# Kernel optimization log

Hardware: AMD Instinct MI355X
Metric: run time of the kernel (lower is better)

Reference implementation:

```python
import jax, jax.numpy as jnp
import numpy as np

N = 20000      # atoms
E = 320000     # edges
G = 16         # graphs
NEL = 4        # chemical elements
M0 = 64        # 0e channels
M1 = 32        # 1o channels
NB = 8         # Bessel basis
L = 2          # conv layers
HID = 64       # radial MLP hidden
RMAX = 4.0
RIN = RMAX - 0.5
NNB = 16.0     # n_neighbors normalization


def _bessel(r):
    # Bessel radial embedding with smooth cosine cutoff between RIN and RMAX
    r_safe = jnp.maximum(r, 1e-6)
    n = jnp.arange(1, NB + 1, dtype=r.dtype)
    f = jnp.sqrt(2.0 / RMAX) * jnp.sin(n[None, :] * jnp.pi * r_safe[:, None] / RMAX) / r_safe[:, None]
    t = (r - RIN) / (RMAX - RIN)
    env = jnp.where(r < RIN, 1.0, jnp.where(r > RMAX, 0.0, 0.5 * (jnp.cos(jnp.pi * t) + 1.0)))
    return f * env[:, None]


def _conv(s, v, attrs, sh0, sh1, src, dst, remb, Wscs, Wscv, W1s, W1v, R0, R1, R2, W2s, W2v):
    # self-connection: FC tensor product of node features with scalar species attrs
    sc_s = jnp.einsum('ni,ne,ieo->no', s, attrs, Wscs) / np.sqrt(M0 * NEL)    # [N, M0+M1]
    sc_v = jnp.einsum('nic,ne,ieo->noc', v, attrs, Wscv) / np.sqrt(M1 * NEL)  # [N, M1, 3]
    # irrep-wise linear (channel mixing)
    s1 = s @ W1s / np.sqrt(M0)
    v1 = jnp.einsum('nic,io->noc', v, W1v) / np.sqrt(M1)
    # gather to edges
    se, ve = s1[src], v1[src]
    # radial MLP -> per-edge tensor-product weights (2*M0 + 2*M1 = 192)
    w = jax.nn.silu(remb @ R0 / np.sqrt(NB))
    w = jax.nn.silu(w @ R1 / np.sqrt(HID))
    w = w @ R2 / np.sqrt(HID)
    w1, w2, w3, w4 = w[:, :M0], w[:, M0:2 * M0], w[:, 2 * M0:2 * M0 + M1], w[:, 2 * M0 + M1:]
    # CG tensor product paths (uvu): 0e*0e->0e, 1o*1o->0e, 0e*1o->1o, 1o*0e->1o
    m_s = jnp.concatenate([
        w1 * se * sh0[:, None],
        w4 * jnp.einsum('eic,ec->ei', ve, sh1) / np.sqrt(3.0),
    ], axis=1)                                                   # [E, M0+M1]
    m_v = jnp.concatenate([
        (w2 * se)[:, :, None] * sh1[:, None, :],
        (w3 * sh0[:, None])[:, :, None] * ve,
    ], axis=1)                                                   # [E, M0+M1, 3]
    # scatter-sum aggregation
    a_s = jax.ops.segment_sum(m_s, dst, num_segments=N) / np.sqrt(NNB)
    a_v = jax.ops.segment_sum(m_v, dst, num_segments=N) / np.sqrt(NNB)
    # linear back to hidden irreps (+ gate scalars) and self-connection
    o_s = a_s @ W2s / np.sqrt(M0 + M1) + sc_s                    # [N, M0+M1]
    o_v = jnp.einsum('nic,io->noc', a_v, W2v) / np.sqrt(M0 + M1) + sc_v
    # gate nonlinearity: silu on scalars, silu-gates on vectors
    gate = jax.nn.silu(o_s[:, M0:])
    return jax.nn.silu(o_s[:, :M0]), o_v * gate[:, :, None]


def _forward(nodes, dR, senders, receivers, n_node, W_embed, W_sc_s, W_sc_v, W_l1_s, W_l1_v,
             Wr0, Wr1, Wr2, W_l2_s, W_l2_v, W_en1, W_en2, W_mag1, W_mag2,
             scale_occ, shift_occ, energy_scale, energy_shift):
    r = jnp.linalg.norm(dR, axis=-1)
    u = dR / jnp.maximum(r, 1e-6)[:, None]
    sh0 = jnp.ones_like(r)                 # Y0 (component norm)
    sh1 = np.sqrt(3.0) * u                 # Y1 (component norm)
    remb = _bessel(r)                      # [E, NB]
    s = nodes @ W_embed / np.sqrt(NEL)     # initial scalar embedding
    v = jnp.zeros((N, M1, 3), dtype=s.dtype)
    for l in range(L):
        s, v = _conv(s, v, nodes, sh0, sh1, senders, receivers, remb,
                     W_sc_s[l], W_sc_v[l], W_l1_s[l], W_l1_v[l],
                     Wr0[l], Wr1[l], Wr2[l], W_l2_s[l], W_l2_v[l])
    # energy readout
    h_en = s @ W_en1 / np.sqrt(M0)
    atomic = h_en @ W_en2 / np.sqrt(M0 // 2)
    atomic = energy_scale * atomic + energy_shift
    gidx = jnp.repeat(jnp.arange(G), n_node, total_repeat_length=N)
    energy = jax.ops.segment_sum(atomic, gidx, num_segments=G)   # [G, 1]
    # magnetization readout
    h_mag = s @ W_mag1 / np.sqrt(M0)
    mags = h_mag @ W_mag2 / np.sqrt(M0 // 2)                     # [N, 2]
    mags = (nodes[:, :-1] @ scale_occ) * mags + (nodes[:, :-1] @ shift_occ)
    return energy, mags


def setup_inputs() -> dict:
    key = jax.random.key(0)
    ks = jax.random.split(key, 30)
    f = jnp.float32
    inp = {
        'nodes': jax.random.uniform(ks[0], (N, NEL), dtype=f),
        'dR': jax.random.normal(ks[1], (E, 3), dtype=f),
        'senders': jax.random.randint(ks[2], (E,), 0, N, dtype=jnp.int32),
        'receivers': jax.random.randint(ks[3], (E,), 0, N, dtype=jnp.int32),
        'n_node': jnp.full((G,), N // G, dtype=jnp.int32),
        'W_embed': jax.random.normal(ks[4], (NEL, M0), dtype=f),
        'W_sc_s': jax.random.normal(ks[5], (L, M0, NEL, M0 + M1), dtype=f),
        'W_sc_v': jax.random.normal(ks[6], (L, M1, NEL, M1), dtype=f),
        'W_l1_s': jax.random.normal(ks[7], (L, M0, M0), dtype=f),
        'W_l1_v': jax.random.normal(ks[8], (L, M1, M1), dtype=f),
        'Wr0': jax.random.normal(ks[9], (L, NB, HID), dtype=f),
        'Wr1': jax.random.normal(ks[10], (L, HID, HID), dtype=f),
        'Wr2': jax.random.normal(ks[11], (L, HID, 2 * M0 + 2 * M1), dtype=f),
        'W_l2_s': jax.random.normal(ks[12], (L, M0 + M1, M0 + M1), dtype=f),
        'W_l2_v': jax.random.normal(ks[13], (L, M0 + M1, M1), dtype=f),
        'W_en1': jax.random.normal(ks[14], (M0, M0 // 2), dtype=f),
        'W_en2': jax.random.normal(ks[15], (M0 // 2, 1), dtype=f),
        'W_mag1': jax.random.normal(ks[16], (M0, M0 // 2), dtype=f),
        'W_mag2': jax.random.normal(ks[17], (M0 // 2, 2), dtype=f),
        'scale_occ': jax.random.uniform(ks[18], (NEL - 1, 2), dtype=f),
        'shift_occ': jax.random.normal(ks[19], (NEL - 1, 2), dtype=f),
        'energy_scale': jnp.ones((), dtype=f),
        'energy_shift': jnp.zeros((), dtype=f),
    }
    return inp


def reference(nodes, dR, senders, receivers, n_node, W_embed, W_sc_s, W_sc_v, W_l1_s, W_l1_v,
              Wr0, Wr1, Wr2, W_l2_s, W_l2_v, W_en1, W_en2, W_mag1, W_mag2,
              scale_occ, shift_occ, energy_scale, energy_shift):
    return _forward(nodes, dR, senders, receivers, n_node, W_embed, W_sc_s, W_sc_v, W_l1_s, W_l1_v,
                    Wr0, Wr1, Wr2, W_l2_s, W_l2_v, W_en1, W_en2, W_mag1, W_mag2,
                    scale_occ, shift_occ, energy_scale, energy_shift)
```

## Files before the change

### kernel.cpp

```cpp
#include <hip/hip_runtime.h>
#include <hip/hip_fp16.h>
#include <math.h>

#define NN 20000
#define NE 320000
#define NG 16
#define ECAP 48

typedef _Float16 f16x2 __attribute__((ext_vector_type(2)));
typedef _Float16 f16x8 __attribute__((ext_vector_type(8)));
typedef float    f32x4 __attribute__((ext_vector_type(4)));

__device__ __forceinline__ float dot2f(f16x2 a, f16x2 b, float c){
#if defined(__has_builtin)
#if __has_builtin(__builtin_amdgcn_fdot2)
  return __builtin_amdgcn_fdot2(a, b, c, false);
#else
  return c + (float)a.x*(float)b.x + (float)a.y*(float)b.y;
#endif
#else
  return c + (float)a.x*(float)b.x + (float)a.y*(float)b.y;
#endif
}

__device__ __forceinline__ f16x2 pack2f(float a, float b){
  f16x2 r; r.x = (_Float16)a; r.y = (_Float16)b; return r;
}

__device__ __forceinline__ float silu_f(float x){ return x / (1.0f + __expf(-x)); }

__device__ __forceinline__ void bessel8(const float* __restrict__ dR, int e, float* rb){
  float x = dR[3*e+0], y = dR[3*e+1], z = dR[3*e+2];
  float r = sqrtf(x*x + y*y + z*z);
  float rs = fmaxf(r, 1e-6f);
  float inv = 1.0f / rs;
  float env;
  if (r < 3.5f) env = 1.0f;
  else if (r > 4.0f) env = 0.0f;
  else {
    float t = (r - 3.5f) * 2.0f;
    env = 0.5f * (cosf(3.14159265358979323846f * t) + 1.0f);
  }
  float c = 0.7071067811865476f * inv * env;
  #pragma unroll
  for (int k=0;k<8;k++){
    float arg = (float)(k+1) * 0.7853981633974483f * rs;
    rb[k] = c * sinf(arg);
  }
}

__global__ void k_geom(const float* __restrict__ dR, float* __restrict__ sh1){
  int e = blockIdx.x*256 + threadIdx.x;
  if (e >= NE) return;
  float x = dR[3*e+0], y = dR[3*e+1], z = dR[3*e+2];
  float r = sqrtf(x*x + y*y + z*z);
  float inv = 1.0f / fmaxf(r, 1e-6f);
  const float SQ3 = 1.7320508075688772f;
  sh1[3*e+0] = SQ3 * x * inv;
  sh1[3*e+1] = SQ3 * y * inv;
  sh1[3*e+2] = SQ3 * z * inv;
}

__global__ void k_prep(const float* __restrict__ dR, const int* __restrict__ senders,
                       const int* __restrict__ perm,
                       float* __restrict__ sh1, float* __restrict__ dRp,
                       int* __restrict__ sendp){
  int p = blockIdx.x*256 + threadIdx.x;
  if (p >= NE) return;
  int e = perm[p];
  float x = dR[3*e+0], y = dR[3*e+1], z = dR[3*e+2];
  dRp[3*p+0] = x; dRp[3*p+1] = y; dRp[3*p+2] = z;
  float r = sqrtf(x*x + y*y + z*z);
  float inv = 1.0f / fmaxf(r, 1e-6f);
  const float SQ3 = 1.7320508075688772f;
  sh1[3*p+0] = SQ3 * x * inv;
  sh1[3*p+1] = SQ3 * y * inv;
  sh1[3*p+2] = SQ3 * z * inv;
  sendp[p] = senders[e];
}

__global__ void k_wt(const float* __restrict__ Wscs, const float* __restrict__ Wscv,
                     float* __restrict__ Wst, float* __restrict__ Wvt){
  int idx = blockIdx.x*256 + threadIdx.x;
  if (idx < 49152){
    int l = idx/24576, r = idx - l*24576;
    int i = r/384; int rem = r - i*384; int e = rem/96; int o = rem - e*96;
    Wst[l*24576 + i*384 + o*4 + e] = Wscs[idx];
  } else if (idx < 49152 + 8192){
    int k = idx - 49152;
    int l = k/4096, r = k - l*4096;
    int i = r/128; int rem = r - i*128; int e = rem/32; int op = rem - e*32;
    Wvt[l*4096 + i*128 + op*4 + e] = Wscv[idx];
  }
}

__global__ void k_embed(const float* __restrict__ nodes, const float* __restrict__ W,
                        float* __restrict__ s){
  int idx = blockIdx.x*256 + threadIdx.x;
  int n = idx>>6, o = idx&63;
  float a = nodes[n*4+0]*W[o] + nodes[n*4+1]*W[64+o]
          + nodes[n*4+2]*W[128+o] + nodes[n*4+3]*W[192+o];
  s[idx] = 0.5f*a;
}

__global__ void k_hist(const int* __restrict__ receivers, int* __restrict__ cnt){
  int e = blockIdx.x*256 + threadIdx.x;
  if (e < NE) atomicAdd(&cnt[receivers[e]], 1);
}

__global__ void k_scan(const int* __restrict__ cnt, int* __restrict__ row, int* __restrict__ cur){
  __shared__ int lsum[1024];
  int t = threadIdx.x;
  int base = t*20;
  int local[20];
  int s = 0;
  #pragma unroll
  for (int i=0;i<20;i++){
    int idx = base+i;
    int v = (idx<NN) ? cnt[idx] : 0;
    local[i] = s; s += v;
  }
  lsum[t] = s; __syncthreads();
  for (int off=1; off<1024; off<<=1){
    int v = (t>=off) ? lsum[t-off] : 0;
    __syncthreads();
    lsum[t] += v;
    __syncthreads();
  }
  int pre = (t>0) ? lsum[t-1] : 0;
  #pragma unroll
  for (int i=0;i<20;i++){
    int idx = base+i;
    if (idx<NN){ int r = pre+local[i]; row[idx]=r; cur[idx]=r; }
  }
  if (t==1023) row[NN] = lsum[1023];
}

__global__ void k_scatter(const int* __restrict__ receivers, int* __restrict__ cur,
                          int* __restrict__ perm){
  int e = blockIdx.x*256 + threadIdx.x;
  if (e < NE){
    int d = receivers[e];
    int p = atomicAdd(&cur[d], 1);
    perm[p] = e;
  }
}

__global__ void k_node(const float* __restrict__ s, const float* __restrict__ v,
                       const float* __restrict__ attrs,
                       const float* __restrict__ W1s, const float* __restrict__ W1v,
                       const float* __restrict__ Wscst, const float* __restrict__ Wscvt,
                       __half* __restrict__ s1, __half* __restrict__ v1,
                       float* __restrict__ scs, float* __restrict__ scv){
  __shared__ float ls[16][64];
  __shared__ float lv[16][96];
  __shared__ float la[16][4];
  int tid = threadIdx.x;
  int nb = blockIdx.x*16;
  for (int i=tid;i<1024;i+=256) ls[i>>6][i&63] = s[(size_t)(nb+(i>>6))*64 + (i&63)];
  for (int i=tid;i<1536;i+=256){ int j=i/96, q=i-96*j; lv[j][q] = v[(size_t)(nb+j)*96+q]; }
  if (tid<64) la[tid>>2][tid&3] = attrs[(nb+(tid>>2))*4 + (tid&3)];
  __syncthreads();
  int w = tid>>6, q = tid&63;
  int jb = w*4;
  float laj[4][4];
  #pragma unroll
  for (int j=0;j<4;j++)
    #pragma unroll
    for (int e=0;e<4;e++) laj[j][e] = la[jb+j][e];

  {
    float acc[4] = {0,0,0,0};
    for (int i=0;i<64;i++){
      float wv = W1s[i*64+q];
      #pragma unroll
      for (int j=0;j<4;j++) acc[j] = fmaf(ls[jb+j][i], wv, acc[j]);
    }
    #pragma unroll
    for (int j=0;j<4;j++) s1[(size_t)(nb+jb+j)*64+q] = __float2half(acc[j]*0.125f);
  }
  #pragma unroll 1
  for (int o=q;o<96;o+=64){
    float t0[4]={0,0,0,0}, t1[4]={0,0,0,0}, t2[4]={0,0,0,0}, t3[4]={0,0,0,0};
    for (int i=0;i<64;i++){
      float4 wv4 = *(const float4*)(Wscst + i*384 + o*4);
      #pragma unroll
      for (int j=0;j<4;j++){
        float sv = ls[jb+j][i];
        t0[j] = fmaf(sv, wv4.x, t0[j]);
        t1[j] = fmaf(sv, wv4.y, t1[j]);
        t2[j] = fmaf(sv, wv4.z, t2[j]);
        t3[j] = fmaf(sv, wv4.w, t3[j]);
      }
    }
    #pragma unroll
    for (int j=0;j<4;j++){
      float acc = t0[j]*laj[j][0] + t1[j]*laj[j][1]
                + t2[j]*laj[j][2] + t3[j]*laj[j][3];
      scs[(size_t)(nb+jb+j)*96+o] = acc*0.0625f;
    }
  }
  #pragma unroll 1
  for (int f=q;f<96;f+=64){
    int op=f/3, c=f-3*op;
    float acc[4] = {0,0,0,0};
    for (int i=0;i<32;i++){
      float wv = W1v[i*32+op];
      #pragma unroll
      for (int j=0;j<4;j++) acc[j] = fmaf(lv[jb+j][i*3+c], wv, acc[j]);
    }
    #pragma unroll
    for (int j=0;j<4;j++) v1[(size_t)(nb+jb+j)*96+f] = __float2half(acc[j]*0.17677669529663687f);
  }
  #pragma unroll 1
  for (int f=q;f<96;f+=64){
    int op=f/3, c=f-3*op;
    float t0[4]={0,0,0,0}, t1[4]={0,0,0,0}, t2[4]={0,0,0,0}, t3[4]={0,0,0,0};
    for (int i=0;i<32;i++){
      float4 wv4 = *(const float4*)(Wscvt + i*128 + op*4);
      #pragma unroll
      for (int j=0;j<4;j++){
        float vv = lv[jb+j][i*3+c];
        t0[j] = fmaf(vv, wv4.x, t0[j]);
        t1[j] = fmaf(vv, wv4.y, t1[j]);
        t2[j] = fmaf(vv, wv4.z, t2[j]);
        t3[j] = fmaf(vv, wv4.w, t3[j]);
      }
    }
    #pragma unroll
    for (int j=0;j<4;j++){
      float acc = t0[j]*laj[j][0] + t1[j]*laj[j][1]
                + t2[j]*laj[j][2] + t3[j]*laj[j][3];
      scv[(size_t)(nb+jb+j)*96+f] = acc*0.08838834764831845f;
    }
  }
}

#define R2S 196
#define HT2S 68
__launch_bounds__(256, 3)
__global__ void k_edgew(const float* __restrict__ dRp,
                        const int* __restrict__ row, int n0, int n1, int cap,
                        const float* __restrict__ R0, const float* __restrict__ R1,
                        const float* __restrict__ R2,
                        __half* __restrict__ wbuf){
  __shared__ __align__(16) f16x2 hT2[32*HT2S];
  __shared__ __align__(16) float r0s[512];
  __shared__ __align__(16) f16x2 wgt1[32*HT2S];
  __shared__ __align__(16) f16x2 wgt2[32*R2S];
  int tid = threadIdx.x;
  int p0 = row[n0], p1 = row[n1];
  int vmax = p1 - p0; if (vmax > cap) vmax = cap;
  int ntiles = (vmax + 63) >> 6;

  if (tid < 128) ((float4*)r0s)[tid] = ((const float4*)R0)[tid];
  for (int i=tid; i<2048; i+=256){
    int kp = i>>6, j = i&63;
    wgt1[kp*HT2S + j] = pack2f(R1[(2*kp)*64 + j], R1[(2*kp+1)*64 + j]);
  }
  for (int i=tid; i<6144; i+=256){
    int kp = i/192, o = i-192*kp;
    wgt2[kp*R2S + o] = pack2f(R2[(2*kp)*192 + o], R2[(2*kp+1)*192 + o]);
  }

  int eg = tid & 15, e0 = eg*4;
  int jg = tid >> 4, j0 = jg*4;
  int wv = tid >> 6;
  int ln = tid & 63;
  int col = ln & 15;
  int quad = ln >> 4;

  for (int tile = blockIdx.x; tile < ntiles; tile += gridDim.x){
    int tbase = tile*64;
    int vcnt = vmax - tbase; if (vcnt > 64) vcnt = 64;

    __syncthreads();
    float* hTf = (float*)hT2;
    if (tid < 64){
      float rbv[8];
      if (tid < vcnt){
        bessel8(dRp, p0 + tbase + tid, rbv);
      } else {
        #pragma unroll
        for (int k=0;k<8;k++) rbv[k]=0.0f;
      }
      #pragma unroll
      for (int k=0;k<8;k++) hTf[k*HT2S + tid] = rbv[k];
    }
    __syncthreads();

    float rb[8][4];
    {
      const float4* hTf4 = (const float4*)hTf;
      #pragma unroll
      for (int k=0;k<8;k++){
        float4 v = hTf4[k*17 + eg];
        rb[k][0]=v.x; rb[k][1]=v.y; rb[k][2]=v.z; rb[k][3]=v.w;
      }
    }
    float a[4][4];
    #pragma unroll
    for (int j=0;j<4;j++)
      #pragma unroll
      for (int e=0;e<4;e++) a[j][e]=0.0f;
    {
      const float4* r0s4 = (const float4*)r0s;
      #pragma unroll
      for (int k=0;k<8;k++){
        float4 w = r0s4[k*16 + jg];
        float wj[4] = {w.x,w.y,w.z,w.w};
        #pragma unroll
        for (int j=0;j<4;j++)
          #pragma unroll
          for (int e=0;e<4;e++) a[j][e] = fmaf(rb[k][e], wj[j], a[j][e]);
      }
    }
    #pragma unroll
    for (int j=0;j<4;j++)
      #pragma unroll
      for (int e=0;e<4;e++) a[j][e] = silu_f(a[j][e]*0.3535533905932738f);
    __syncthreads();
    #pragma unroll
    for (int jp=0;jp<2;jp++){
      union {uint4 u; f16x2 h[4];} U;
      #pragma unroll
      for (int e=0;e<4;e++) U.h[e] = pack2f(a[2*jp][e], a[2*jp+1][e]);
      *(uint4*)(hT2 + (j0/2 + jp)*HT2S + e0) = U.u;
    }
    __syncthreads();

    {
      const unsigned int* hT2u = (const unsigned int*)hT2;
      const unsigned int* wgt1u = (const unsigned int*)wgt1;
      union { uint4 u; f16x8 v; } A0, A1;
      int jA = 16*wv + col;
      A0.u.x = wgt1u[(4*quad+0)*HT2S + jA];
      A0.u.y = wgt1u[(4*quad+1)*HT2S + jA];
      A0.u.z = wgt1u[(4*quad+2)*HT2S + jA];
      A0.u.w = wgt1u[(4*quad+3)*HT2S + jA];
      A1.u.x = wgt1u[(16+4*quad+0)*HT2S + jA];
      A1.u.y = wgt1u[(16+4*quad+1)*HT2S + jA];
      A1.u.z = wgt1u[(16+4*quad+2)*HT2S + jA];
      A1.u.w = wgt1u[(16+4*quad+3)*HT2S + jA];
      f32x4 accB[4];
      #pragma unroll
      for (int nt=0; nt<4; nt++){
        union { uint4 u; f16x8 v; } B0, B1;
        int eB = 16*nt + col;
        B0.u.x = hT2u[(4*quad+0)*HT2S + eB];
        B0.u.y = hT2u[(4*quad+1)*HT2S + eB];
        B0.u.z = hT2u[(4*quad+2)*HT2S + eB];
        B0.u.w = hT2u[(4*quad+3)*HT2S + eB];
        B1.u.x = hT2u[(16+4*quad+0)*HT2S + eB];
        B1.u.y = hT2u[(16+4*quad+1)*HT2S + eB];
        B1.u.z = hT2u[(16+4*quad+2)*HT2S + eB];
        B1.u.w = hT2u[(16+4*quad+3)*HT2S + eB];
        f32x4 acc = {0.0f,0.0f,0.0f,0.0f};
        acc = __builtin_amdgcn_mfma_f32_16x16x32_f16(A0.v, B0.v, acc, 0, 0, 0);
        acc = __builtin_amdgcn_mfma_f32_16x16x32_f16(A1.v, B1.v, acc, 0, 0, 0);
        accB[nt] = acc;
      }
      __syncthreads();
      #pragma unroll
      for (int nt=0; nt<4; nt++){
        float h0 = silu_f(accB[nt][0]*0.125f);
        float h1v = silu_f(accB[nt][1]*0.125f);
        float h2v = silu_f(accB[nt][2]*0.125f);
        float h3v = silu_f(accB[nt][3]*0.125f);
        hT2[(8*wv + 2*quad + 0)*HT2S + 16*nt + col] = pack2f(h0, h1v);
        hT2[(8*wv + 2*quad + 1)*HT2S + 16*nt + col] = pack2f(h2v, h3v);
      }
    }
    __syncthreads();

    {
      const unsigned int* hT2u = (const unsigned int*)hT2;
      const unsigned int* wgt2u = (const unsigned int*)wgt2;
      int eA = 16*wv + col;
      union { uint4 u; f16x8 v; } A0, A1;
      A0.u.x = hT2u[(4*quad+0)*HT2S + eA];
      A0.u.y = hT2u[(4*quad+1)*HT2S + eA];
      A0.u.z = hT2u[(4*quad+2)*HT2S + eA];
      A0.u.w = hT2u[(4*quad+3)*HT2S + eA];
      A1.u.x = hT2u[(16+4*quad+0)*HT2S + eA];
      A1.u.y = hT2u[(16+4*quad+1)*HT2S + eA];
      A1.u.z = hT2u[(16+4*quad+2)*HT2S + eA];
      A1.u.w = hT2u[(16+4*quad+3)*HT2S + eA];
      int erow = 16*wv + 4*quad;
      #pragma unroll
      for (int ot=0; ot<12; ot++){
        int o = 16*ot + col;
        union { uint4 u; f16x8 v; } B0, B1;
        B0.u.x = wgt2u[(4*quad+0)*R2S + o];
        B0.u.y = wgt2u[(4*quad+1)*R2S + o];
        B0.u.z = wgt2u[(4*quad+2)*R2S + o];
        B0.u.w = wgt2u[(4*quad+3)*R2S + o];
        B1.u.x = wgt2u[(16+4*quad+0)*R2S + o];
        B1.u.y = wgt2u[(16+4*quad+1)*R2S + o];
        B1.u.z = wgt2u[(16+4*quad+2)*R2S + o];
        B1.u.w = wgt2u[(16+4*quad+3)*R2S + o];
        f32x4 acc = {0.0f,0.0f,0.0f,0.0f};
        acc = __builtin_amdgcn_mfma_f32_16x16x32_f16(A0.v, B0.v, acc, 0, 0, 0);
        acc = __builtin_amdgcn_mfma_f32_16x16x32_f16(A1.v, B1.v, acc, 0, 0, 0);
        #pragma unroll
        for (int r=0;r<4;r++){
          int eib = erow + r;
          if (eib < vcnt)
            wbuf[(size_t)(tbase+eib)*192 + o] = __float2half(acc[r]);
        }
      }
    }
  }
}

__launch_bounds__(128, 4)
__global__ void k_gather(const __half* __restrict__ wbuf,
                         const int* __restrict__ row, const int* __restrict__ sendp,
                         const float* __restrict__ sh1,
                         const __half* __restrict__ s1, const __half* __restrict__ v1,
                         int n0, int cap,
                         float* __restrict__ a_s, float* __restrict__ a_v){
  __shared__ int   srcs[ECAP];
  __shared__ float sh1r[ECAP*3];
  int n = n0 + blockIdx.x;
  int t = threadIdx.x;
  int pc0 = row[n0];
  int p0 = row[n], p1 = row[n+1];
  int pmax = pc0 + cap; if (p1 > pmax) p1 = pmax;

  int iv = (t - 64) >> 1;
  bool even = ((t & 1) == 0);

  float acs = 0.0f, av0 = 0.0f, av1 = 0.0f, av2 = 0.0f;

  for (int base = p0; base < p1; base += ECAP){
    int bc = p1 - base; if (bc > ECAP) bc = ECAP;
    __syncthreads();
    if (t < bc){
      srcs[t] = sendp[base + t];
      sh1r[3*t+0] = sh1[3*(base+t)+0];
      sh1r[3*t+1] = sh1[3*(base+t)+1];
      sh1r[3*t+2] = sh1[3*(base+t)+2];
    }
    __syncthreads();
    const __half* wb = wbuf + (size_t)(base - pc0)*192;
    if (t < 64){
      int o = t;
      int j = 0;
      for (; j + 8 <= bc; j += 8){
        float sv[8], w1[8], w2[8];
        #pragma unroll
        for (int u=0;u<8;u++){
          const __half* wr = wb + (j+u)*192;
          sv[u] = __half2float(s1[(size_t)srcs[j+u]*64 + o]);
          w1[u] = __half2float(wr[o]);
          w2[u] = __half2float(wr[64 + o]);
        }
        #pragma unroll
        for (int u=0;u<8;u++){
          acs = fmaf(w1[u], sv[u], acs);
          float uu = w2[u] * sv[u];
          av0 = fmaf(uu, sh1r[3*(j+u)+0], av0);
          av1 = fmaf(uu, sh1r[3*(j+u)+1], av1);
          av2 = fmaf(uu, sh1r[3*(j+u)+2], av2);
        }
      }
      for (; j < bc; ++j){
        const __half* wr = wb + j*192;
        float sv = __half2float(s1[(size_t)srcs[j]*64 + o]);
        float w1v = __half2float(wr[o]);
        float w2v = __half2float(wr[64 + o]);
        acs = fmaf(w1v, sv, acs);
        float uu = w2v * sv;
        av0 = fmaf(uu, sh1r[3*j+0], av0);
        av1 = fmaf(uu, sh1r[3*j+1], av1);
        av2 = fmaf(uu, sh1r[3*j+2], av2);
      }
    } else {
      int j = 0;
      for (; j + 8 <= bc; j += 8){
        float v0[8], vc1[8], vc2[8], w3[8], w4[8];
        #pragma unroll
        for (int u=0;u<8;u++){
          const __half* wr = wb + (j+u)*192;
          const __half* vr = v1 + (size_t)srcs[j+u]*96 + 3*iv;
          v0[u]  = __half2float(vr[0]);
          vc1[u] = __half2float(vr[1]);
          vc2[u] = __half2float(vr[2]);
          w3[u]  = __half2float(wr[128 + iv]);
          w4[u]  = __half2float(wr[160 + iv]);
        }
        #pragma unroll
        for (int u=0;u<8;u++){
          if (even){
            float dv = v0[u]*sh1r[3*(j+u)+0] + vc1[u]*sh1r[3*(j+u)+1] + vc2[u]*sh1r[3*(j+u)+2];
            acs = fmaf(w4[u], dv, acs);
            av0 = fmaf(w3[u], v0[u], av0);
          } else {
            av1 = fmaf(w3[u], vc1[u], av1);
            av2 = fmaf(w3[u], vc2[u], av2);
          }
        }
      }
      for (; j < bc; ++j){
        const __half* wr = wb + j*192;
        const __half* vr = v1 + (size_t)srcs[j]*96 + 3*iv;
        float v0 = __half2float(vr[0]);
        float vc1 = __half2float(vr[1]);
        float vc2 = __half2float(vr[2]);
        float w3 = __half2float(wr[128 + iv]);
        if (even){
          float w4 = __half2float(wr[160 + iv]);
          float dv = v0*sh1r[3*j+0] + vc1*sh1r[3*j+1] + vc2*sh1r[3*j+2];
          acs = fmaf(w4, dv, acs);
          av0 = fmaf(w3, v0, av0);
        } else {
          av1 = fmaf(w3, vc1, av1);
          av2 = fmaf(w3, vc2, av2);
        }
      }
    }
  }

  if (t < 64){
    a_s[(size_t)n*96 + t] = 0.03125f*acs;
    a_v[(size_t)n*288 + 3*t + 0] = 0.03125f*av0;
    a_v[(size_t)n*288 + 3*t + 1] = 0.03125f*av1;
    a_v[(size_t)n*288 + 3*t + 2] = 0.03125f*av2;
  } else if (even){
    a_s[(size_t)n*96 + 64 + iv] = 0.018042195912175807f*acs;
    a_v[(size_t)n*288 + 192 + 3*iv + 0] = 0.03125f*av0;
  } else {
    a_v[(size_t)n*288 + 192 + 3*iv + 1] = 0.03125f*av1;
    a_v[(size_t)n*288 + 192 + 3*iv + 2] = 0.03125f*av2;
  }
}

__device__ __forceinline__ void mlp_h2(const float* __restrict__ R0,
                                       const float* lR1, const float rb[8],
                                       float h2[64]){
  float h1[64];
  #pragma unroll
  for (int j=0;j<64;j+=4){
    float a0=0,a1=0,a2=0,a3=0;
    #pragma unroll
    for (int k=0;k<8;k++){
      float r = rb[k];
      const float* wp = R0 + k*64 + j;
      a0 = fmaf(r, wp[0], a0); a1 = fmaf(r, wp[1], a1);
      a2 = fmaf(r, wp[2], a2); a3 = fmaf(r, wp[3], a3);
    }
    h1[j+0]=silu_f(a0*0.3535533905932738f);
    h1[j+1]=silu_f(a1*0.3535533905932738f);
    h1[j+2]=silu_f(a2*0.3535533905932738f);
    h1[j+3]=silu_f(a3*0.3535533905932738f);
  }
  #pragma unroll
  for (int j=0;j<64;j+=4){
    float a0=0,a1=0,a2=0,a3=0;
    #pragma unroll
    for (int k=0;k<64;k++){
      float h = h1[k];
      float4 w4 = *(const float4*)(lR1 + k*64 + j);
      a0 = fmaf(h,w4.x,a0); a1 = fmaf(h,w4.y,a1);
      a2 = fmaf(h,w4.z,a2); a3 = fmaf(h,w4.w,a3);
    }
    h2[j+0]=silu_f(a0*0.125f);
    h2[j+1]=silu_f(a1*0.125f);
    h2[j+2]=silu_f(a2*0.125f);
    h2[j+3]=silu_f(a3*0.125f);
  }
}

__launch_bounds__(256, 2)
__global__ void k_edge(const float* __restrict__ dR, const float* __restrict__ sh1,
                       const int* __restrict__ senders, const int* __restrict__ receivers,
                       const __half* __restrict__ s1, const __half* __restrict__ v1,
                       const float* __restrict__ R0, const float* __restrict__ R1,
                       const float* __restrict__ R2,
                       float* __restrict__ a_s, float* __restrict__ a_v){
  __shared__ __align__(16) float lR1[64*64];
  __shared__ __align__(16) float lR2[64*192];
  int tid = threadIdx.x;
  for (int i=tid;i<4096;i+=256)  lR1[i]=R1[i];
  for (int i=tid;i<12288;i+=256) lR2[i]=R2[i];
  __syncthreads();
  int e = blockIdx.x*256 + tid;
  float rb[8];
  bessel8(dR, e, rb);
  float h2[64];
  mlp_h2(R0, lR1, rb, h2);
  int src = senders[e], dst = receivers[e];
  float sx=sh1[3*e+0], sy=sh1[3*e+1], sz=sh1[3*e+2];
  const __half* srow = s1 + (size_t)src*64;
  const __half* vrow = v1 + (size_t)src*96;
  float* asr = a_s + (size_t)dst*96;
  float* avr = a_v + (size_t)dst*288;
  #pragma unroll 1
  for (int o=0;o<64;o+=4){
    float w10=0,w11=0,w12=0,w13=0, w20=0,w21=0,w22=0,w23=0;
    #pragma unroll
    for (int k=0;k<64;k++){
      float h = h2[k];
      float4 wa = *(const float4*)(lR2 + k*192 + o);
      float4 wb = *(const float4*)(lR2 + k*192 + 64 + o);
      w10=fmaf(h,wa.x,w10); w11=fmaf(h,wa.y,w11); w12=fmaf(h,wa.z,w12); w13=fmaf(h,wa.w,w13);
      w20=fmaf(h,wb.x,w20); w21=fmaf(h,wb.y,w21); w22=fmaf(h,wb.z,w22); w23=fmaf(h,wb.w,w23);
    }
    float sev[4] = {__half2float(srow[o+0]), __half2float(srow[o+1]),
                    __half2float(srow[o+2]), __half2float(srow[o+3])};
    float w1a[4] = {w10,w11,w12,w13};
    float w2a[4] = {w20,w21,w22,w23};
    #pragma unroll
    for (int u=0;u<4;u++){
      atomicAdd(asr+o+u, 0.03125f*w1a[u]*sev[u]);
      float m = 0.03125f*w2a[u]*sev[u];
      atomicAdd(avr+(o+u)*3+0, m*sx);
      atomicAdd(avr+(o+u)*3+1, m*sy);
      atomicAdd(avr+(o+u)*3+2, m*sz);
    }
  }
  #pragma unroll 1
  for (int i0=0;i0<32;i0+=4){
    float w30=0,w31=0,w32=0,w33=0, w40=0,w41=0,w42=0,w43=0;
    #pragma unroll
    for (int k=0;k<64;k++){
      float h = h2[k];
      float4 wa = *(const float4*)(lR2 + k*192 + 128 + i0);
      float4 wb = *(const float4*)(lR2 + k*192 + 160 + i0);
      w30=fmaf(h,wa.x,w30); w31=fmaf(h,wa.y,w31); w32=fmaf(h,wa.z,w32); w33=fmaf(h,wa.w,w33);
      w40=fmaf(h,wb.x,w40); w41=fmaf(h,wb.y,w41); w42=fmaf(h,wb.z,w42); w43=fmaf(h,wb.w,w43);
    }
    float w3a[4] = {w30,w31,w32,w33};
    float w4a[4] = {w40,w41,w42,w43};
    #pragma unroll
    for (int u=0;u<4;u++){
      int i = i0+u;
      float vx=__half2float(vrow[3*i+0]), vy=__half2float(vrow[3*i+1]), vz=__half2float(vrow[3*i+2]);
      float dv = vx*sx + vy*sy + vz*sz;
      atomicAdd(asr+64+i, 0.018042195912175807f*w4a[u]*dv);
      float m3 = 0.03125f*w3a[u];
      atomicAdd(avr+(64+i)*3+0, m3*vx);
      atomicAdd(avr+(64+i)*3+1, m3*vy);
      atomicAdd(avr+(64+i)*3+2, m3*vz);
    }
  }
}

__launch_bounds__(256, 4)
__global__ void k_out(const float* __restrict__ a_s, const float* __restrict__ a_v,
                      const float* __restrict__ scs, const float* __restrict__ scv,
                      const float* __restrict__ W2s, const float* __restrict__ W2v,
                      float* __restrict__ s_out, float* __restrict__ v_out){
  __shared__ float las[16][96];
  __shared__ float lav[16][288];
  __shared__ float los[16][96];
  int tid = threadIdx.x;
  int nb = blockIdx.x*16;
  for (int i=tid;i<1536;i+=256){ int j=i/96,  q=i-96*j;  las[j][q] = a_s[(size_t)(nb+j)*96 +q]; }
  for (int i=tid;i<4608;i+=256){ int j=i/288, q=i-288*j; lav[j][q] = a_v[(size_t)(nb+j)*288+q]; }
  __syncthreads();
  int w = tid>>6, q = tid&63;
  int jb = w*4;

  #pragma unroll 1
  for (int o=q; o<96; o+=64){
    float acc[4] = {0,0,0,0};
    for (int i=0;i<96;i++){
      float wv = W2s[i*96+o];
      #pragma unroll
      for (int j=0;j<4;j++) acc[j] = fmaf(las[jb+j][i], wv, acc[j]);
    }
    #pragma unroll
    for (int j=0;j<4;j++)
      los[jb+j][o] = acc[j]*0.10206207261596575f + scs[(size_t)(nb+jb+j)*96+o];
  }
  __syncthreads();

  #pragma unroll
  for (int j=0;j<4;j++) s_out[(size_t)(nb+jb+j)*64+q] = silu_f(los[jb+j][q]);

  #pragma unroll 1
  for (int f=q; f<96; f+=64){
    int op=f/3, c=f-3*op;
    float acc[4] = {0,0,0,0};
    for (int i=0;i<96;i++){
      float wv = W2v[i*32+op];
      #pragma unroll
      for (int j=0;j<4;j++) acc[j] = fmaf(lav[jb+j][i*3+c], wv, acc[j]);
    }
    #pragma unroll
    for (int j=0;j<4;j++){
      float ov = acc[j]*0.10206207261596575f + scv[(size_t)(nb+jb+j)*96+f];
      float g = silu_f(los[jb+j][64+op]);
      v_out[(size_t)(nb+jb+j)*96+f] = ov*g;
    }
  }
}

__global__ void k_final(const float* __restrict__ s, const float* __restrict__ nodes,
                        const int* __restrict__ n_node,
                        const float* __restrict__ Wen1, const float* __restrict__ Wen2,
                        const float* __restrict__ Wm1, const float* __restrict__ Wm2,
                        const float* __restrict__ scale_occ, const float* __restrict__ shift_occ,
                        const float* __restrict__ escale, const float* __restrict__ eshift,
                        float* __restrict__ out){
  __shared__ float eacc[NG];
  __shared__ int goff[NG+1];
  int tid = threadIdx.x;
  if (tid < NG) eacc[tid] = 0.0f;
  if (tid == 0){
    int c = 0; goff[0] = 0;
    for (int g=0; g<NG; g++){ c += n_node[g]; goff[g+1] = c; }
  }
  __syncthreads();
  int n = blockIdx.x*256 + tid;
  if (n < NN){
    float sv[64];
    #pragma unroll
    for (int i=0;i<64;i++) sv[i]=s[(size_t)n*64+i];
    float en=0.0f, m0=0.0f, m1=0.0f;
    #pragma unroll 1
    for (int jj=0;jj<32;jj++){
      float he=0.0f, hm=0.0f;
      #pragma unroll
      for (int i=0;i<64;i++){
        he = fmaf(sv[i], Wen1[i*32+jj], he);
        hm = fmaf(sv[i], Wm1[i*32+jj], hm);
      }
      he *= 0.125f; hm *= 0.125f;
      en = fmaf(he, Wen2[jj], en);
      m0 = fmaf(hm, Wm2[jj*2+0], m0);
      m1 = fmaf(hm, Wm2[jj*2+1], m1);
    }
    const float INVS32 = 0.17677669529663687f;
    en *= INVS32; m0 *= INVS32; m1 *= INVS32;
    en = escale[0]*en + eshift[0];
    int g = 0;
    for (int gg=0; gg<NG; gg++) if (n >= goff[gg+1]) g = gg+1;
    atomicAdd(&eacc[g], en);
    float nx=nodes[n*4+0], ny=nodes[n*4+1], nz=nodes[n*4+2];
    float sc0 = nx*scale_occ[0] + ny*scale_occ[2] + nz*scale_occ[4];
    float sc1 = nx*scale_occ[1] + ny*scale_occ[3] + nz*scale_occ[5];
    float sf0 = nx*shift_occ[0] + ny*shift_occ[2] + nz*shift_occ[4];
    float sf1 = nx*shift_occ[1] + ny*shift_occ[3] + nz*shift_occ[5];
    out[16 + n*2 + 0] = sc0*m0 + sf0;
    out[16 + n*2 + 1] = sc1*m1 + sf1;
  }
  __syncthreads();
  if (tid < NG) atomicAdd(&out[tid], eacc[tid]);
}

extern "C" void kernel_launch(void* const* d_in, const int* in_sizes, int n_in,
                              void* d_out, int out_size, void* d_ws, size_t ws_size,
                              hipStream_t stream){
  const float* nodes   = (const float*)d_in[0];
  const float* dR      = (const float*)d_in[1];
  const int*  senders  = (const int*)d_in[2];
  const int*  receivers= (const int*)d_in[3];
  const int*  n_node   = (const int*)d_in[4];
  const float* W_embed = (const float*)d_in[5];
  const float* W_sc_s  = (const float*)d_in[6];
  const float* W_sc_v  = (const float*)d_in[7];
  const float* W_l1_s  = (const float*)d_in[8];
  const float* W_l1_v  = (const float*)d_in[9];
  const float* Wr0     = (const float*)d_in[10];
  const float* Wr1     = (const float*)d_in[11];
  const float* Wr2     = (const float*)d_in[12];
  const float* W_l2_s  = (const float*)d_in[13];
  const float* W_l2_v  = (const float*)d_in[14];
  const float* W_en1   = (const float*)d_in[15];
  const float* W_en2   = (const float*)d_in[16];
  const float* W_mag1  = (const float*)d_in[17];
  const float* W_mag2  = (const float*)d_in[18];
  const float* scale_occ = (const float*)d_in[19];
  const float* shift_occ = (const float*)d_in[20];
  const float* escale  = (const float*)d_in[21];
  const float* eshift  = (const float*)d_in[22];
  float* out = (float*)d_out;
  float* ws  = (float*)d_ws;

  float*  sh1  = ws + 0;
  float*  sA   = ws + 960000;
  float*  vA   = ws + 2240000;
  __half* s1h  = (__half*)(ws + 4160000);
  __half* v1h  = (__half*)(ws + 4800000);
  float*  dRp  = ws + 5760000;
  int*    sendp= (int*)(ws + 6720000);
  float*  Wst  = ws + 7040000;
  float*  Wvt  = ws + 7089152;
  float*  scs  = ws + 7360000;
  float*  scv  = ws + 9280000;
  float*  a_s  = ws + 11200000;
  float*  a_v  = ws + 13120000;
  int*    cnt  = (int*)(ws + 18880000);
  int*    row  = (int*)(ws + 18900000);
  int*    cur  = (int*)(ws + 18920004);
  int*    perm = (int*)(ws + 18940004);
  __half* wbuf = (__half*)(ws + 19260008);

  size_t wsf = ws_size / 4;
  size_t cap_edges = (wsf > 19260008) ? ((wsf - 19260008)*4) / 384 : 0;
  if (cap_edges > 128) cap_edges -= 64;
  const bool fast = cap_edges >= 4096;
  int cap = (int)((cap_edges > (size_t)NE) ? (size_t)NE + 8192 : cap_edges);
  int npc;
  if (cap_edges > (size_t)NE){
    npc = NN;
  } else {
    npc = (int)(cap / 20); if (npc < 1) npc = 1; if (npc > NN) npc = NN;
  }
  int nchunk = (NN + npc - 1) / npc;

  hipMemsetAsync(vA, 0, (size_t)NN*96*sizeof(float), stream);
  hipMemsetAsync(out, 0, 16*sizeof(float), stream);

  k_embed<<<5000, 256, 0, stream>>>(nodes, W_embed, sA);
  k_wt<<<225, 256, 0, stream>>>(W_sc_s, W_sc_v, Wst, Wvt);

  if (fast){
    hipMemsetAsync(cnt, 0, NN*sizeof(int), stream);
    k_hist<<<1250, 256, 0, stream>>>(receivers, cnt);
    k_scan<<<1, 1024, 0, stream>>>(cnt, row, cur);
    k_scatter<<<1250, 256, 0, stream>>>(receivers, cur, perm);
    k_prep<<<1250, 256, 0, stream>>>(dR, senders, perm, sh1, dRp, sendp);
  } else {
    k_geom<<<1250, 256, 0, stream>>>(dR, sh1);
  }

  for (int l=0; l<2; l++){
    k_node<<<1250, 256, 0, stream>>>(sA, vA, nodes,
                                     W_l1_s + l*4096, W_l1_v + l*1024,
                                     Wst + l*24576, Wvt + l*4096,
                                     s1h, v1h, scs, scv);
    if (fast){
      for (int ck=0; ck<nchunk; ck++){
        int n0 = ck*npc;
        int n1 = n0 + npc; if (n1 > NN) n1 = NN;
        int cover = (n1-n0)*17 + 4096; if (cover > cap) cover = cap;
        int ntile_ub = (cover+63)/64;
        int grid = ntile_ub < 768 ? ntile_ub : 768;
        k_edgew<<<grid, 256, 0, stream>>>(dRp, row, n0, n1, cap,
                                       Wr0 + l*512, Wr1 + l*4096, Wr2 + l*12288, wbuf);
        k_gather<<<n1-n0, 128, 0, stream>>>(wbuf, row, sendp, sh1, s1h, v1h,
                                            n0, cap, a_s, a_v);
      }
    } else {
      hipMemsetAsync(a_s, 0, (size_t)NN*384*sizeof(float), stream);
      k_edge<<<1250, 256, 0, stream>>>(dR, sh1, senders, receivers, s1h, v1h,
                                       Wr0 + l*512, Wr1 + l*4096, Wr2 + l*12288,
                                       a_s, a_v);
    }
    k_out<<<1250, 256, 0, stream>>>(a_s, a_v, scs, scv,
                                    W_l2_s + l*9216, W_l2_v + l*3072,
                                    sA, vA);
  }
  k_final<<<79, 256, 0, stream>>>(sA, nodes, n_node, W_en1, W_en2, W_mag1, W_mag2,
                                  scale_occ, shift_occ, escale, eshift, out);
}
```

Baseline: 597.5 us.

## Keep radial MLP layer-1 MFMA weights in registers and raise edge-kernel occupancy

In the edge-weight kernel, the R1 weights for the second MLP layer now go straight into per-lane MFMA A-operand registers, loaded once per block. The shared-memory copy and the per-tile LDS reads are gone, which frees LDS. That lets launch bounds go from 3 to 4 blocks per SM and the grid cap rise from 768 to 1024. The node kernel's inner loops are also manually unrolled by 4 to batch weight loads. The risks are register pressure from the extra waves and a mismatch in the A-operand k-index packing (8*quad instead of the previous 4*quad pair layout), which must match the B layout.

```diff
diff --git a/kernel.cpp b/kernel.cpp
--- a/kernel.cpp
+++ b/kernel.cpp
@@ -25,6 +25,10 @@
 
 __device__ __forceinline__ f16x2 pack2f(float a, float b){
   f16x2 r; r.x = (_Float16)a; r.y = (_Float16)b; return r;
+}
+
+__device__ __forceinline__ unsigned packu2f(float a, float b){
+  union { f16x2 h; unsigned u; } X; X.h = pack2f(a, b); return X.u;
 }
 
 __device__ __forceinline__ float silu_f(float x){ return x / (1.0f + __expf(-x)); }
@@ -171,10 +175,18 @@
 
   {
     float acc[4] = {0,0,0,0};
-    for (int i=0;i<64;i++){
-      float wv = W1s[i*64+q];
-      #pragma unroll
-      for (int j=0;j<4;j++) acc[j] = fmaf(ls[jb+j][i], wv, acc[j]);
+    for (int i=0;i<64;i+=4){
+      float wv0 = W1s[(i+0)*64+q];
+      float wv1 = W1s[(i+1)*64+q];
+      float wv2 = W1s[(i+2)*64+q];
+      float wv3 = W1s[(i+3)*64+q];
+      #pragma unroll
+      for (int j=0;j<4;j++){
+        acc[j] = fmaf(ls[jb+j][i+0], wv0, acc[j]);
+        acc[j] = fmaf(ls[jb+j][i+1], wv1, acc[j]);
+        acc[j] = fmaf(ls[jb+j][i+2], wv2, acc[j]);
+        acc[j] = fmaf(ls[jb+j][i+3], wv3, acc[j]);
+      }
     }
     #pragma unroll
     for (int j=0;j<4;j++) s1[(size_t)(nb+jb+j)*64+q] = __float2half(acc[j]*0.125f);
@@ -182,15 +194,23 @@
   #pragma unroll 1
   for (int o=q;o<96;o+=64){
     float t0[4]={0,0,0,0}, t1[4]={0,0,0,0}, t2[4]={0,0,0,0}, t3[4]={0,0,0,0};
-    for (int i=0;i<64;i++){
-      float4 wv4 = *(const float4*)(Wscst + i*384 + o*4);
+    for (int i=0;i<64;i+=4){
+      float4 wa = *(const float4*)(Wscst + (i+0)*384 + o*4);
+      float4 wb = *(const float4*)(Wscst + (i+1)*384 + o*4);
+      float4 wc = *(const float4*)(Wscst + (i+2)*384 + o*4);
+      float4 wd = *(const float4*)(Wscst + (i+3)*384 + o*4);
       #pragma unroll
       for (int j=0;j<4;j++){
-        float sv = ls[jb+j][i];
-        t0[j] = fmaf(sv, wv4.x, t0[j]);
-        t1[j] = fmaf(sv, wv4.y, t1[j]);
-        t2[j] = fmaf(sv, wv4.z, t2[j]);
-        t3[j] = fmaf(sv, wv4.w, t3[j]);
+        float s0 = ls[jb+j][i+0], s1v = ls[jb+j][i+1];
+        float s2 = ls[jb+j][i+2], s3 = ls[jb+j][i+3];
+        t0[j] = fmaf(s0, wa.x, t0[j]); t1[j] = fmaf(s0, wa.y, t1[j]);
+        t2[j] = fmaf(s0, wa.z, t2[j]); t3[j] = fmaf(s0, wa.w, t3[j]);
+        t0[j] = fmaf(s1v, wb.x, t0[j]); t1[j] = fmaf(s1v, wb.y, t1[j]);
+        t2[j] = fmaf(s1v, wb.z, t2[j]); t3[j] = fmaf(s1v, wb.w, t3[j]);
+        t0[j] = fmaf(s2, wc.x, t0[j]); t1[j] = fmaf(s2, wc.y, t1[j]);
+        t2[j] = fmaf(s2, wc.z, t2[j]); t3[j] = fmaf(s2, wc.w, t3[j]);
+        t0[j] = fmaf(s3, wd.x, t0[j]); t1[j] = fmaf(s3, wd.y, t1[j]);
+        t2[j] = fmaf(s3, wd.z, t2[j]); t3[j] = fmaf(s3, wd.w, t3[j]);
       }
     }
     #pragma unroll
@@ -204,10 +224,18 @@
   for (int f=q;f<96;f+=64){
     int op=f/3, c=f-3*op;
     float acc[4] = {0,0,0,0};
-    for (int i=0;i<32;i++){
-      float wv = W1v[i*32+op];
-      #pragma unroll
-      for (int j=0;j<4;j++) acc[j] = fmaf(lv[jb+j][i*3+c], wv, acc[j]);
+    for (int i=0;i<32;i+=4){
+      float wv0 = W1v[(i+0)*32+op];
+      float wv1 = W1v[(i+1)*32+op];
+      float wv2 = W1v[(i+2)*32+op];
+      float wv3 = W1v[(i+3)*32+op];
+      #pragma unroll
+      for (int j=0;j<4;j++){
+        acc[j] = fmaf(lv[jb+j][(i+0)*3+c], wv0, acc[j]);
+        acc[j] = fmaf(lv[jb+j][(i+1)*3+c], wv1, acc[j]);
+        acc[j] = fmaf(lv[jb+j][(i+2)*3+c], wv2, acc[j]);
+        acc[j] = fmaf(lv[jb+j][(i+3)*3+c], wv3, acc[j]);
+      }
     }
     #pragma unroll
     for (int j=0;j<4;j++) v1[(size_t)(nb+jb+j)*96+f] = __float2half(acc[j]*0.17677669529663687f);
@@ -216,15 +244,23 @@
   for (int f=q;f<96;f+=64){
     int op=f/3, c=f-3*op;
     float t0[4]={0,0,0,0}, t1[4]={0,0,0,0}, t2[4]={0,0,0,0}, t3[4]={0,0,0,0};
-    for (int i=0;i<32;i++){
-      float4 wv4 = *(const float4*)(Wscvt + i*128 + op*4);
+    for (int i=0;i<32;i+=4){
+      float4 wa = *(const float4*)(Wscvt + (i+0)*128 + op*4);
+      float4 wb = *(const float4*)(Wscvt + (i+1)*128 + op*4);
+      float4 wc = *(const float4*)(Wscvt + (i+2)*128 + op*4);
+      float4 wd = *(const float4*)(Wscvt + (i+3)*128 + op*4);
       #pragma unroll
       for (int j=0;j<4;j++){
-        float vv = lv[jb+j][i*3+c];
-        t0[j] = fmaf(vv, wv4.x, t0[j]);
-        t1[j] = fmaf(vv, wv4.y, t1[j]);
-        t2[j] = fmaf(vv, wv4.z, t2[j]);
-        t3[j] = fmaf(vv, wv4.w, t3[j]);
+        float v0 = lv[jb+j][(i+0)*3+c], v1v = lv[jb+j][(i+1)*3+c];
+        float v2 = lv[jb+j][(i+2)*3+c], v3 = lv[jb+j][(i+3)*3+c];
+        t0[j] = fmaf(v0, wa.x, t0[j]); t1[j] = fmaf(v0, wa.y, t1[j]);
+        t2[j] = fmaf(v0, wa.z, t2[j]); t3[j] = fmaf(v0, wa.w, t3[j]);
+        t0[j] = fmaf(v1v, wb.x, t0[j]); t1[j] = fmaf(v1v, wb.y, t1[j]);
+        t2[j] = fmaf(v1v, wb.z, t2[j]); t3[j] = fmaf(v1v, wb.w, t3[j]);
+        t0[j] = fmaf(v2, wc.x, t0[j]); t1[j] = fmaf(v2, wc.y, t1[j]);
+        t2[j] = fmaf(v2, wc.z, t2[j]); t3[j] = fmaf(v2, wc.w, t3[j]);
+        t0[j] = fmaf(v3, wd.x, t0[j]); t1[j] = fmaf(v3, wd.y, t1[j]);
+        t2[j] = fmaf(v3, wd.z, t2[j]); t3[j] = fmaf(v3, wd.w, t3[j]);
       }
     }
     #pragma unroll
@@ -238,7 +274,7 @@
 
 #define R2S 196
 #define HT2S 68
-__launch_bounds__(256, 3)
+__launch_bounds__(256, 4)
 __global__ void k_edgew(const float* __restrict__ dRp,
                         const int* __restrict__ row, int n0, int n1, int cap,
                         const float* __restrict__ R0, const float* __restrict__ R1,
@@ -246,22 +282,11 @@
                         __half* __restrict__ wbuf){
   __shared__ __align__(16) f16x2 hT2[32*HT2S];
   __shared__ __align__(16) float r0s[512];
-  __shared__ __align__(16) f16x2 wgt1[32*HT2S];
   __shared__ __align__(16) f16x2 wgt2[32*R2S];
   int tid = threadIdx.x;
   int p0 = row[n0], p1 = row[n1];
   int vmax = p1 - p0; if (vmax > cap) vmax = cap;
   int ntiles = (vmax + 63) >> 6;
-
-  if (tid < 128) ((float4*)r0s)[tid] = ((const float4*)R0)[tid];
-  for (int i=tid; i<2048; i+=256){
-    int kp = i>>6, j = i&63;
-    wgt1[kp*HT2S + j] = pack2f(R1[(2*kp)*64 + j], R1[(2*kp+1)*64 + j]);
-  }
-  for (int i=tid; i<6144; i+=256){
-    int kp = i/192, o = i-192*kp;
-    wgt2[kp*R2S + o] = pack2f(R2[(2*kp)*192 + o], R2[(2*kp+1)*192 + o]);
-  }
 
   int eg = tid & 15, e0 = eg*4;
   int jg = tid >> 4, j0 = jg*4;
@@ -269,6 +294,24 @@
   int ln = tid & 63;
   int col = ln & 15;
   int quad = ln >> 4;
+
+  if (tid < 128) ((float4*)r0s)[tid] = ((const float4*)R0)[tid];
+  for (int i=tid; i<6144; i+=256){
+    int kp = i/192, o = i-192*kp;
+    wgt2[kp*R2S + o] = pack2f(R2[(2*kp)*192 + o], R2[(2*kp+1)*192 + o]);
+  }
+  union { uint4 u; f16x8 v; } rA0, rA1;
+  {
+    int jA = 16*wv + col;
+    rA0.u.x = packu2f(R1[(8*quad+0)*64 + jA], R1[(8*quad+1)*64 + jA]);
+    rA0.u.y = packu2f(R1[(8*quad+2)*64 + jA], R1[(8*quad+3)*64 + jA]);
+    rA0.u.z = packu2f(R1[(8*quad+4)*64 + jA], R1[(8*quad+5)*64 + jA]);
+    rA0.u.w = packu2f(R1[(8*quad+6)*64 + jA], R1[(8*quad+7)*64 + jA]);
+    rA1.u.x = packu2f(R1[(32+8*quad+0)*64 + jA], R1[(32+8*quad+1)*64 + jA]);
+    rA1.u.y = packu2f(R1[(32+8*quad+2)*64 + jA], R1[(32+8*quad+3)*64 + jA]);
+    rA1.u.z = packu2f(R1[(32+8*quad+4)*64 + jA], R1[(32+8*quad+5)*64 + jA]);
+    rA1.u.w = packu2f(R1[(32+8*quad+6)*64 + jA], R1[(32+8*quad+7)*64 + jA]);
+  }
 
   for (int tile = blockIdx.x; tile < ntiles; tile += gridDim.x){
     int tbase = tile*64;
@@ -331,17 +374,6 @@
 
     {
       const unsigned int* hT2u = (const unsigned int*)hT2;
-      const unsigned int* wgt1u = (const unsigned int*)wgt1;
-      union { uint4 u; f16x8 v; } A0, A1;
-      int jA = 16*wv + col;
-      A0.u.x = wgt1u[(4*quad+0)*HT2S + jA];
-      A0.u.y = wgt1u[(4*quad+1)*HT2S + jA];
-      A0.u.z = wgt1u[(4*quad+2)*HT2S + jA];
-      A0.u.w = wgt1u[(4*quad+3)*HT2S + jA];
-      A1.u.x = wgt1u[(16+4*quad+0)*HT2S + jA];
-      A1.u.y = wgt1u[(16+4*quad+1)*HT2S + jA];
-      A1.u.z = wgt1u[(16+4*quad+2)*HT2S + jA];
-      A1.u.w = wgt1u[(16+4*quad+3)*HT2S + jA];
       f32x4 accB[4];
       #pragma unroll
       for (int nt=0; nt<4; nt++){
@@ -356,8 +388,8 @@
         B1.u.z = hT2u[(16+4*quad+2)*HT2S + eB];
         B1.u.w = hT2u[(16+4*quad+3)*HT2S + eB];
         f32x4 acc = {0.0f,0.0f,0.0f,0.0f};
-        acc = __builtin_amdgcn_mfma_f32_16x16x32_f16(A0.v, B0.v, acc, 0, 0, 0);
-        acc = __builtin_amdgcn_mfma_f32_16x16x32_f16(A1.v, B1.v, acc, 0, 0, 0);
+        acc = __builtin_amdgcn_mfma_f32_16x16x32_f16(rA0.v, B0.v, acc, 0, 0, 0);
+        acc = __builtin_amdgcn_mfma_f32_16x16x32_f16(rA1.v, B1.v, acc, 0, 0, 0);
         accB[nt] = acc;
       }
       __syncthreads();
@@ -839,7 +871,7 @@
         int n1 = n0 + npc; if (n1 > NN) n1 = NN;
         int cover = (n1-n0)*17 + 4096; if (cover > cap) cover = cap;
         int ntile_ub = (cover+63)/64;
-        int grid = ntile_ub < 768 ? ntile_ub : 768;
+        int grid = ntile_ub < 1024 ? ntile_ub : 1024;
         k_edgew<<<grid, 256, 0, stream>>>(dRp, row, n0, n1, cap,
                                        Wr0 + l*512, Wr1 + l*4096, Wr2 + l*12288, wbuf);
         k_gather<<<n1-n0, 128, 0, stream>>>(wbuf, row, sendp, sh1, s1h, v1h,
```

New measurement: 591.3 us, median of 2. About the same (-1.0%).
